# Kernel tuning notes

Measured on AMD Instinct MI355X. Metric: run time of the kernel, lower is better.

Reference implementation:

```python
import jax, jax.numpy as jnp
import numpy as np

B, H, W, C = 2, 48, 96, 128
N = H * W
NH, HD = 8, 32
WIN_R = 1
WLEN = 2 * WIN_R + 2
ATTN_NUM = WLEN * WLEN
FIELD_DIM = 2
D_SELF = C + FIELD_DIM + NH * 2   # 146
E_SELF = D_SELF + 1               # 147 (noc embed)
D_CROSS = C + FIELD_DIM           # 130
ATTN_DIM = NH * HD                # 256
HID = C * 2                       # ConvGLU hidden
SCALE = HD ** -0.5


def init_coords():
    gx, gy = jnp.meshgrid(jnp.arange(W, dtype=jnp.float32), jnp.arange(H, dtype=jnp.float32))
    return jnp.stack([gx, gy], axis=-1)[None]  # [1,H,W,2] (x,y)


def layer_norm(x, g, b, eps=1e-5):
    mu = x.mean(-1, keepdims=True)
    var = ((x - mu) ** 2).mean(-1, keepdims=True)
    return (x - mu) * jax.lax.rsqrt(var + eps) * g + b


def swap_halves(t):
    a, b = jnp.split(t, 2, axis=0)
    return jnp.concatenate([b, a], axis=0)


def bilinear_sample(img, coords):
    # img [B,H,W,C]; coords [B,H,W,2] absolute (x,y)
    x = jnp.clip(coords[..., 0], 0.0, W - 1.0)
    y = jnp.clip(coords[..., 1], 0.0, H - 1.0)
    x0 = jnp.clip(jnp.floor(x), 0, W - 2).astype(jnp.int32); x1 = x0 + 1
    y0 = jnp.clip(jnp.floor(y), 0, H - 2).astype(jnp.int32); y1 = y0 + 1
    wx = (x - x0)[..., None]; wy = (y - y0)[..., None]
    bi = jnp.arange(img.shape[0])[:, None, None]
    v00 = img[bi, y0, x0]; v01 = img[bi, y0, x1]
    v10 = img[bi, y1, x0]; v11 = img[bi, y1, x1]
    return (1 - wy) * ((1 - wx) * v00 + wx * v01) + wy * ((1 - wx) * v10 + wx * v11)


def consistency_mask(field, A=2.0):
    offset = field + init_coords()
    f_t2r = bilinear_sample(swap_halves(field), offset)
    diff = jnp.abs(field + f_t2r).sum(-1, keepdims=True)
    return (diff < A).astype(field.dtype)  # [B,H,W,1]


def match_attention_core(q, k, v, max_offset):
    # q,k,v: [B,N,NH,HD]; max_offset: [B,N,NH,2] absolute (x,y)
    r = WIN_R
    ox = jnp.clip(max_offset[..., 0], float(r), W - 1 - r - 0.001)
    oy = jnp.clip(max_offset[..., 1], float(r), H - 1 - r - 0.001)
    mxf = jnp.floor(ox); myf = jnp.floor(oy)
    fx = (ox - mxf).transpose(0, 2, 1)[..., None, None]  # [B,NH,N,1,1]
    fy = (oy - myf).transpose(0, 2, 1)[..., None, None]
    mx = mxf.astype(jnp.int32).transpose(0, 2, 1)  # [B,NH,N]
    my = myf.astype(jnp.int32).transpose(0, 2, 1)
    qh = q.transpose(0, 2, 1, 3); kh = k.transpose(0, 2, 1, 3); vh = v.transpose(0, 2, 1, 3)
    dxs = jnp.arange(WLEN) - r                    # window: floor-r .. floor+r+1
    gx = mx[..., None] + dxs                      # [B,NH,N,WLEN]
    gy = my[..., None] + dxs
    idx = (gy[..., :, None] * W + gx[..., None, :]).reshape(B, NH, N, ATTN_NUM)
    bi = jnp.arange(B)[:, None, None, None]
    hi = jnp.arange(NH)[None, :, None, None]
    kg = kh[bi, hi, idx]                          # [B,NH,N,ATTN_NUM,HD]
    s = jnp.einsum('bhnd,bhnad->bhna', qh, kg) * SCALE
    S = s.reshape(B, NH, N, WLEN, WLEN)           # [..., y, x]
    w00 = (1 - fy) * (1 - fx); w01 = (1 - fy) * fx; w10 = fy * (1 - fx); w11 = fy * fx
    # continuous (2r+1)^2 window scores by bilinear interp of integer-grid scores
    s_cont = (w00 * S[..., :-1, :-1] + w01 * S[..., :-1, 1:]
              + w10 * S[..., 1:, :-1] + w11 * S[..., 1:, 1:])
    p = jax.nn.softmax(s_cont.reshape(B, NH, N, -1), axis=-1).reshape(s_cont.shape)
    # scatter continuous probs back to the (2r+2)^2 integer grid with bilinear weights
    Ag = jnp.zeros((B, NH, N, WLEN, WLEN), p.dtype)
    Ag = Ag.at[..., :-1, :-1].add(w00 * p)
    Ag = Ag.at[..., :-1, 1:].add(w01 * p)
    Ag = Ag.at[..., 1:, :-1].add(w10 * p)
    Ag = Ag.at[..., 1:, 1:].add(w11 * p)
    Af = Ag.reshape(B, NH, N, ATTN_NUM)
    vg = vh[bi, hi, idx]                          # [B,NH,N,ATTN_NUM,HD]
    out = jnp.einsum('bhna,bhnad->bhnd', Af, vg)
    return out.transpose(0, 2, 1, 3).reshape(B, N, ATTN_DIM), Af.transpose(0, 2, 1, 3)


def reference(x, self_rpos, field, field_scale, n0_g, n0_b, n1_g, n1_b, n2_g, n2_b,
              sq_w, sk_w, sv_w, sp_w, cq_w, ck_w, cv_w, cg_w, cp_w,
              fc1_w, fc1_b, dw_w, dw_b, fc2_w, fc2_b):
    noc = consistency_mask(jax.lax.stop_gradient(field))
    xc = jnp.concatenate([x, field * field_scale, self_rpos], axis=-1)  # [B,H,W,D_SELF]
    coords0 = jnp.tile(init_coords(), (1, 1, 1, NH))  # [1,H,W,2*NH]
    self_off = (self_rpos + coords0).reshape(B, N, NH, 2)
    # --- self MatchAttention (noc_embed) ---
    h0 = layer_norm(xc, n0_g, n0_b).reshape(B, N, D_SELF)
    xe = jnp.concatenate([h0, noc.reshape(B, N, 1)], axis=-1)
    q = (xe @ sq_w).reshape(B, N, NH, HD)
    k = (xe @ sk_w).reshape(B, N, NH, HD)
    v = (xe @ sv_w).reshape(B, N, NH, HD)
    o, _ = match_attention_core(q, k, v, self_off)
    xc = xc + (o @ sp_w).reshape(B, H, W, D_SELF)
    self_rpos_out = xc[..., -NH * 2:]
    xc = xc[..., :D_CROSS]
    xc = xc.at[..., -1].set(0.0)  # stereo: zero y-flow
    field1 = xc[..., -FIELD_DIM:] / field_scale
    off = (jnp.tile(field1, (1, 1, 1, NH)) + coords0).reshape(B, N, NH, 2)
    # --- cross MatchAttention ---
    h1 = layer_norm(xc, n1_g, n1_b).reshape(B, N, D_CROSS)
    ref = h1
    tgt = swap_halves(h1)
    g = jax.nn.silu(ref @ cg_w)
    q = (ref @ cq_w).reshape(B, N, NH, HD)
    k = (tgt @ ck_w).reshape(B, N, NH, HD)
    v = (tgt @ cv_w).reshape(B, N, NH, HD)
    o, attn = match_attention_core(q, k, v, off)
    o = jnp.concatenate([g * o, attn.reshape(B, N, NH * ATTN_NUM)], axis=-1)
    xc = xc + (o @ cp_w).reshape(B, H, W, D_CROSS)
    xc = xc.at[..., -1].set(0.0)
    field2 = xc[..., -FIELD_DIM:] / field_scale
    xo = xc[..., :C]
    # --- ConvGLU MLP ---
    h2 = layer_norm(xo, n2_g, n2_b)
    u = h2 @ fc1_w + fc1_b
    a, gv = jnp.split(u, 2, axis=-1)
    a = jax.lax.conv_general_dilated(a, dw_w, (1, 1), 'SAME',
                                     dimension_numbers=('NHWC', 'HWIO', 'NHWC'),
                                     feature_group_count=HID) + dw_b
    a = jax.nn.gelu(a, approximate=False) * gv
    xo = xo + (a @ fc2_w + fc2_b)
    return xo, self_rpos_out, field2


def setup_inputs() -> dict:
    key = jax.random.key(0)
    ks = jax.random.split(key, 16)
    def rn(i, shape, s=1.0):
        return jax.random.normal(ks[i], shape, dtype=jnp.float32) * s
    return {
        'x': rn(0, (B, H, W, C)),
        'self_rpos': rn(1, (B, H, W, NH * 2)),
        'field': rn(2, (B, H, W, FIELD_DIM)),
        'field_scale': 0.1 * jnp.ones((1, 1, 1, 2), jnp.float32),
        'n0_g': jnp.ones((D_SELF,), jnp.float32), 'n0_b': jnp.zeros((D_SELF,), jnp.float32),
        'n1_g': jnp.ones((D_CROSS,), jnp.float32), 'n1_b': jnp.zeros((D_CROSS,), jnp.float32),
        'n2_g': jnp.ones((C,), jnp.float32), 'n2_b': jnp.zeros((C,), jnp.float32),
        'sq_w': rn(3, (E_SELF, ATTN_DIM), 0.02), 'sk_w': rn(4, (E_SELF, ATTN_DIM), 0.02),
        'sv_w': rn(5, (E_SELF, ATTN_DIM), 0.02), 'sp_w': rn(6, (ATTN_DIM, D_SELF), 0.02),
        'cq_w': rn(7, (D_CROSS, ATTN_DIM), 0.02), 'ck_w': rn(8, (D_CROSS, ATTN_DIM), 0.02),
        'cv_w': rn(9, (D_CROSS, ATTN_DIM), 0.02), 'cg_w': rn(10, (D_CROSS, ATTN_DIM), 0.02),
        'cp_w': rn(11, (ATTN_DIM + NH * ATTN_NUM, D_CROSS), 0.02),
        'fc1_w': rn(12, (C, 2 * HID), 0.02), 'fc1_b': jnp.zeros((2 * HID,), jnp.float32),
        'dw_w': rn(13, (3, 3, 1, HID), 0.1), 'dw_b': jnp.zeros((HID,), jnp.float32),
        'fc2_w': rn(14, (HID, C), 0.02), 'fc2_b': jnp.zeros((C,), jnp.float32),
    }
```

## Files before the change

### kernel.cpp

```cpp
#include <hip/hip_runtime.h>
#include <math.h>

namespace {
constexpr int Bn = 2, Hh = 48, Ww = 96, Cch = 128;
constexpr int Nn = Hh * Ww;
constexpr int NHh = 8;
constexpr int DSELF = 146, ESELF = 147, DCROSS = 130;
constexpr int Mrows = Bn * Nn;
constexpr float SCALEf = 0.17677669529663687f;
}

typedef float f32x4 __attribute__((ext_vector_type(4)));
typedef short s16x8 __attribute__((ext_vector_type(8)));

__device__ __forceinline__ unsigned short f2b(float f) {
  unsigned int u = __float_as_uint(f);
  u = u + 0x7fffu + ((u >> 16) & 1u);
  return (unsigned short)(u >> 16);
}
__device__ __forceinline__ float b2f(unsigned short u) {
  return __uint_as_float((unsigned int)u << 16);
}

__device__ __forceinline__ f32x4 mfma_bf16(s16x8 a, s16x8 b, f32x4 c) {
  f32x4 d;
  asm volatile("v_mfma_f32_16x16x32_bf16 %0, %1, %2, %3"
               : "=&v"(d) : "v"(a), "v"(b), "v"(c));
  return d;
}

__device__ __forceinline__ float wave_bcast_sum(float v) {
#pragma unroll
  for (int off = 32; off > 0; off >>= 1) v += __shfl_down(v, off);
  return __shfl(v, 0);
}

struct WDesc { const float* src; int K, N, Kp, dstOff, blkOff; };
struct WPack { WDesc d[11]; };

__global__ __launch_bounds__(256) void convert_w_kernel(WPack p, unsigned short* dst) {
  int bi = blockIdx.x;
  int mi = 0;
#pragma unroll
  for (int i = 1; i < 11; i++) if (bi >= p.d[i].blkOff) mi = i;
  WDesc w = p.d[mi];
  int e = (bi - w.blkOff) * 2048 + threadIdx.x * 8;
  int total = w.N * w.Kp;
  if (e >= total) return;
  int n = e / w.Kp, k0 = e - n * w.Kp;
  s16x8 pack;
#pragma unroll
  for (int j = 0; j < 8; j++) {
    int kk = k0 + j;
    float vv = (kk < w.K) ? w.src[(size_t)kk * w.N + n] : 0.f;
    pack[j] = (short)f2b(vv);
  }
  *reinterpret_cast<s16x8*>(dst + w.dstOff + e) = pack;
}

__global__ __launch_bounds__(256) void mfma_gemm_kernel(
    const unsigned short* __restrict__ A, int Kp,
    const unsigned short* __restrict__ Wt, int N,
    const float* __restrict__ bias, const float* __restrict__ resid,
    void* __restrict__ out, int swapA, int act, int out_bf16) {
  __shared__ unsigned short As[64 * 40];
  __shared__ unsigned short Bs[64 * 40];
  int tid = threadIdx.x;
  int m0 = blockIdx.y * 64, n0 = blockIdx.x * 64;
  int lane = tid & 63, wv = tid >> 6;
  int wr = wv >> 1, wc = wv & 1;
  int lr = lane & 15, lk = (lane >> 4) * 8;
  int sr = tid >> 2, sk8 = (tid & 3) * 8;
  int am = m0 + sr;
  if (swapA) am = (am < Mrows / 2) ? am + Mrows / 2 : am - Mrows / 2;
  const unsigned short* aptr = A + (size_t)am * Kp + sk8;
  int bn = n0 + sr;
  const unsigned short* bptr = (bn < N) ? Wt + (size_t)bn * Kp + sk8 : nullptr;
  f32x4 acc00 = {}, acc01 = {}, acc10 = {}, acc11 = {};
  for (int k0 = 0; k0 < Kp; k0 += 32) {
    s16x8 av = *reinterpret_cast<const s16x8*>(aptr + k0);
    s16x8 bv = {};
    if (bptr) bv = *reinterpret_cast<const s16x8*>(bptr + k0);
    *reinterpret_cast<s16x8*>(&As[sr * 40 + sk8]) = av;
    *reinterpret_cast<s16x8*>(&Bs[sr * 40 + sk8]) = bv;
    __syncthreads();
    s16x8 a0 = *reinterpret_cast<const s16x8*>(&As[(wr * 32 + lr) * 40 + lk]);
    s16x8 a1 = *reinterpret_cast<const s16x8*>(&As[(wr * 32 + 16 + lr) * 40 + lk]);
    s16x8 b0 = *reinterpret_cast<const s16x8*>(&Bs[(wc * 32 + lr) * 40 + lk]);
    s16x8 b1 = *reinterpret_cast<const s16x8*>(&Bs[(wc * 32 + 16 + lr) * 40 + lk]);
    acc00 = mfma_bf16(a0, b0, acc00);
    acc01 = mfma_bf16(a0, b1, acc01);
    acc10 = mfma_bf16(a1, b0, acc10);
    acc11 = mfma_bf16(a1, b1, acc11);
    __syncthreads();
  }
  int rowBase = m0 + wr * 32 + (lane >> 4) * 4;
  f32x4 accs[2][2] = {{acc00, acc01}, {acc10, acc11}};
#pragma unroll
  for (int fc = 0; fc < 2; fc++) {
    int col = n0 + wc * 32 + fc * 16 + lr;
    if (col >= N) continue;
    float bval = bias ? bias[col] : 0.f;
    bool dosilu = (act == 1) || (act == 2 && col >= 256);
#pragma unroll
    for (int fr = 0; fr < 2; fr++) {
#pragma unroll
      for (int r = 0; r < 4; r++) {
        int row = rowBase + fr * 16 + r;
        float vv = accs[fr][fc][r] + bval;
        if (resid) vv += resid[(size_t)row * N + col];
        if (dosilu) vv = vv / (1.f + expf(-vv));
        if (out_bf16)
          ((unsigned short*)out)[(size_t)row * N + col] = f2b(vv);
        else
          ((float*)out)[(size_t)row * N + col] = vv;
      }
    }
  }
}

__global__ __launch_bounds__(256) void prep_kernel(
    const float* __restrict__ x, const float* __restrict__ rpos,
    const float* __restrict__ field, const float* __restrict__ fs,
    const float* __restrict__ n0g, const float* __restrict__ n0b,
    float* __restrict__ xc, unsigned short* __restrict__ xe_b) {
  int wv = threadIdx.x >> 6, lane = threadIdx.x & 63;
  int pix = blockIdx.x * 4 + wv;
  int b = pix / Nn, n = pix - b * Nn;
  int py = n / Ww, px = n - py * Ww;
  const float* xrow = x + (size_t)pix * Cch;
  const float* rrow = rpos + (size_t)pix * 16;
  float f0 = field[(size_t)pix * 2 + 0], f1 = field[(size_t)pix * 2 + 1];
  float fsx = fs[0], fsy = fs[1];
  float vals[3];
#pragma unroll
  for (int i = 0; i < 3; i++) {
    int c = lane + i * 64;
    float v = 0.f;
    if (c < Cch) v = xrow[c];
    else if (c == 128) v = f0 * fsx;
    else if (c == 129) v = f1 * fsy;
    else if (c < DSELF) v = rrow[c - 130];
    vals[i] = v;
  }
  float* xcrow = xc + (size_t)pix * DSELF;
#pragma unroll
  for (int i = 0; i < 3; i++) {
    int c = lane + i * 64;
    if (c < DSELF) xcrow[c] = vals[i];
  }
  float s = 0.f;
#pragma unroll
  for (int i = 0; i < 3; i++) { int c = lane + i * 64; if (c < DSELF) s += vals[i]; }
  float mu = wave_bcast_sum(s) * (1.f / DSELF);
  float s2 = 0.f;
#pragma unroll
  for (int i = 0; i < 3; i++) {
    int c = lane + i * 64;
    if (c < DSELF) { float d = vals[i] - mu; s2 += d * d; }
  }
  float var = wave_bcast_sum(s2) * (1.f / DSELF);
  float rs = rsqrtf(var + 1e-5f);
  float noc = 0.f;
  if (lane == 0) {
    float ox = fminf(fmaxf(f0 + (float)px, 0.f), (float)(Ww - 1));
    float oy = fminf(fmaxf(f1 + (float)py, 0.f), (float)(Hh - 1));
    float x0f = fminf(fmaxf(floorf(ox), 0.f), (float)(Ww - 2));
    float y0f = fminf(fmaxf(floorf(oy), 0.f), (float)(Hh - 2));
    int x0 = (int)x0f, y0 = (int)y0f;
    float wx = ox - x0f, wy = oy - y0f;
    const float* fo = field + (size_t)(1 - b) * Nn * 2;
    const float* p00 = fo + ((size_t)y0 * Ww + x0) * 2;
    const float* p10 = fo + ((size_t)(y0 + 1) * Ww + x0) * 2;
    float v0 = (1.f - wy) * ((1.f - wx) * p00[0] + wx * p00[2]) +
               wy * ((1.f - wx) * p10[0] + wx * p10[2]);
    float v1 = (1.f - wy) * ((1.f - wx) * p00[1] + wx * p00[3]) +
               wy * ((1.f - wx) * p10[1] + wx * p10[3]);
    float diff = fabsf(f0 + v0) + fabsf(f1 + v1);
    noc = (diff < 2.f) ? 1.f : 0.f;
  }
  noc = __shfl(noc, 0);
  unsigned short* xerow = xe_b + (size_t)pix * 160;
#pragma unroll
  for (int i = 0; i < 3; i++) {
    int c = lane + i * 64;
    if (c < 160) {
      float v;
      if (c < DSELF) v = (vals[i] - mu) * rs * n0g[c] + n0b[c];
      else if (c == 146) v = noc;
      else v = 0.f;
      xerow[c] = f2b(v);
    }
  }
}

__global__ __launch_bounds__(256) void attn_wave_kernel(
    const float* __restrict__ qbuf, int qstride, int gOff,
    const float* __restrict__ kvbuf, int kvstride, int koff, int voff,
    const float* __restrict__ rpos, const float* __restrict__ xc2,
    const float* __restrict__ fs, unsigned short* __restrict__ o, int o_stride,
    int mode) {
  int wv = threadIdx.x >> 6, lane = threadIdx.x & 63;
  int pix = blockIdx.x * 4 + wv;
  int b = pix / Nn, n = pix - b * Nn;
  int py = n / Ww, px = n - py * Ww;
  int h = lane >> 3, c = lane & 7;
  size_t row = (size_t)pix;
  float ox, oy;
  if (mode == 0) {
    ox = rpos[row * 16 + 2 * h] + (float)px;
    oy = rpos[row * 16 + 2 * h + 1] + (float)py;
  } else {
    ox = xc2[row * DCROSS + 128] / fs[0] + (float)px;
    oy = (float)py;
  }
  ox = fminf(fmaxf(ox, 1.0f), 93.999f);
  oy = fminf(fmaxf(oy, 1.0f), 45.999f);
  float mxf = floorf(ox), myf = floorf(oy);
  float fx = ox - mxf, fy = oy - myf;
  int mx = (int)mxf, my = (int)myf;
  int base = b * Nn;

  float4 qv = *reinterpret_cast<const float4*>(qbuf + row * qstride + lane * 4);
  float s[16];
#pragma unroll
  for (int j = 0; j < 4; j++) {
    int gy = my - 1 + j;
#pragma unroll
    for (int i = 0; i < 4; i++) {
      int gx = mx - 1 + i;
      int idx = gy * Ww + gx;
      float4 kv = *reinterpret_cast<const float4*>(
          kvbuf + (size_t)(base + idx) * kvstride + koff + lane * 4);
      float d = qv.x * kv.x + qv.y * kv.y + qv.z * kv.z + qv.w * kv.w;
      d += __shfl_xor(d, 1);
      d += __shfl_xor(d, 2);
      d += __shfl_xor(d, 4);
      s[j * 4 + i] = d * SCALEf;
    }
  }
  float w00 = (1.f - fy) * (1.f - fx), w01 = (1.f - fy) * fx;
  float w10 = fy * (1.f - fx), w11 = fy * fx;
  float sc[9];
#pragma unroll
  for (int j = 0; j < 3; j++)
#pragma unroll
    for (int i = 0; i < 3; i++)
      sc[j * 3 + i] = w00 * s[j * 4 + i] + w01 * s[j * 4 + i + 1] +
                      w10 * s[(j + 1) * 4 + i] + w11 * s[(j + 1) * 4 + i + 1];
  float mval = sc[0];
#pragma unroll
  for (int i = 1; i < 9; i++) mval = fmaxf(mval, sc[i]);
  float p[9], psum = 0.f;
#pragma unroll
  for (int i = 0; i < 9; i++) { p[i] = expf(sc[i] - mval); psum += p[i]; }
  float inv = 1.f / psum;
#pragma unroll
  for (int i = 0; i < 9; i++) p[i] *= inv;
  float Ag[16] = {};
#pragma unroll
  for (int j = 0; j < 3; j++)
#pragma unroll
    for (int i = 0; i < 3; i++) {
      float pv = p[j * 3 + i];
      Ag[j * 4 + i] += w00 * pv;
      Ag[j * 4 + i + 1] += w01 * pv;
      Ag[(j + 1) * 4 + i] += w10 * pv;
      Ag[(j + 1) * 4 + i + 1] += w11 * pv;
    }
  float4 acc = make_float4(0.f, 0.f, 0.f, 0.f);
#pragma unroll
  for (int j = 0; j < 4; j++) {
    int gy = my - 1 + j;
#pragma unroll
    for (int i = 0; i < 4; i++) {
      int gx = mx - 1 + i;
      int idx = gy * Ww + gx;
      float4 vv = *reinterpret_cast<const float4*>(
          kvbuf + (size_t)(base + idx) * kvstride + voff + lane * 4);
      float w = Ag[j * 4 + i];
      acc.x += w * vv.x; acc.y += w * vv.y; acc.z += w * vv.z; acc.w += w * vv.w;
    }
  }
  if (gOff >= 0) {
    float4 gg = *reinterpret_cast<const float4*>(qbuf + row * qstride + gOff + lane * 4);
    acc.x *= gg.x; acc.y *= gg.y; acc.z *= gg.z; acc.w *= gg.w;
  }
  unsigned int p0 = (unsigned int)f2b(acc.x) | ((unsigned int)f2b(acc.y) << 16);
  unsigned int p1 = (unsigned int)f2b(acc.z) | ((unsigned int)f2b(acc.w) << 16);
  *reinterpret_cast<uint2*>(o + row * o_stride + lane * 4) = make_uint2(p0, p1);
  if (mode == 1) {
    float a0 = 0.f, a1 = 0.f;
#pragma unroll
    for (int a = 0; a < 8; a++) {
      if (c == a) { a0 = Ag[2 * a]; a1 = Ag[2 * a + 1]; }
    }
    unsigned int pa = (unsigned int)f2b(a0) | ((unsigned int)f2b(a1) << 16);
    *reinterpret_cast<unsigned int*>(o + row * o_stride + 256 + h * 16 + 2 * c) = pa;
  }
}

__global__ __launch_bounds__(256) void post_self_kernel(
    const float* __restrict__ xcn, const float* __restrict__ n1g,
    const float* __restrict__ n1b, float* __restrict__ out_rpos,
    float* __restrict__ xc2, unsigned short* __restrict__ h1_b) {
  int wv = threadIdx.x >> 6, lane = threadIdx.x & 63;
  int pix = blockIdx.x * 4 + wv;
  const float* row = xcn + (size_t)pix * DSELF;
  float vals[3];
#pragma unroll
  for (int i = 0; i < 3; i++) {
    int c = lane + i * 64;
    vals[i] = (c < DSELF) ? row[c] : 0.f;
  }
#pragma unroll
  for (int i = 0; i < 3; i++) {
    int c = lane + i * 64;
    if (c >= 130 && c < 146) out_rpos[(size_t)pix * 16 + (c - 130)] = vals[i];
  }
#pragma unroll
  for (int i = 0; i < 3; i++) {
    int c = lane + i * 64;
    if (c == 129) vals[i] = 0.f;
  }
  float* x2row = xc2 + (size_t)pix * DCROSS;
#pragma unroll
  for (int i = 0; i < 3; i++) {
    int c = lane + i * 64;
    if (c < DCROSS) x2row[c] = vals[i];
  }
  float s = 0.f;
#pragma unroll
  for (int i = 0; i < 3; i++) { int c = lane + i * 64; if (c < DCROSS) s += vals[i]; }
  float mu = wave_bcast_sum(s) * (1.f / DCROSS);
  float s2 = 0.f;
#pragma unroll
  for (int i = 0; i < 3; i++) {
    int c = lane + i * 64;
    if (c < DCROSS) { float d = vals[i] - mu; s2 += d * d; }
  }
  float var = wave_bcast_sum(s2) * (1.f / DCROSS);
  float rs = rsqrtf(var + 1e-5f);
  unsigned short* h1row = h1_b + (size_t)pix * 160;
#pragma unroll
  for (int i = 0; i < 3; i++) {
    int c = lane + i * 64;
    if (c < 160) {
      float v = (c < DCROSS) ? (vals[i] - mu) * rs * n1g[c] + n1b[c] : 0.f;
      h1row[c] = f2b(v);
    }
  }
}

__global__ __launch_bounds__(256) void post_cross_kernel(
    const float* __restrict__ xc2n, const float* __restrict__ fs,
    const float* __restrict__ n2g, const float* __restrict__ n2b,
    float* __restrict__ out_f2, float* __restrict__ xob,
    unsigned short* __restrict__ h2_b) {
  int wv = threadIdx.x >> 6, lane = threadIdx.x & 63;
  int pix = blockIdx.x * 4 + wv;
  const float* row = xc2n + (size_t)pix * DCROSS;
  float vals[3];
#pragma unroll
  for (int i = 0; i < 3; i++) {
    int c = lane + i * 64;
    vals[i] = (c < DCROSS) ? row[c] : 0.f;
  }
  if (lane == 0) out_f2[(size_t)pix * 2 + 0] = vals[2] / fs[0];
  if (lane == 1) out_f2[(size_t)pix * 2 + 1] = 0.f;
  float* xrow = xob + (size_t)pix * Cch;
#pragma unroll
  for (int i = 0; i < 2; i++) {
    int c = lane + i * 64;
    xrow[c] = vals[i];
  }
  float s = vals[0] + vals[1];
  float mu = wave_bcast_sum(s) * (1.f / Cch);
  float d0 = vals[0] - mu, d1 = vals[1] - mu;
  float var = wave_bcast_sum(d0 * d0 + d1 * d1) * (1.f / Cch);
  float rs = rsqrtf(var + 1e-5f);
  unsigned short* h2row = h2_b + (size_t)pix * Cch;
#pragma unroll
  for (int i = 0; i < 2; i++) {
    int c = lane + i * 64;
    h2row[c] = f2b((vals[i] - mu) * rs * n2g[c] + n2b[c]);
  }
}

__global__ __launch_bounds__(256) void dwconv_kernel(
    const unsigned short* __restrict__ ub, const float* __restrict__ dww,
    const float* __restrict__ dwb, unsigned short* __restrict__ aout) {
  int t = blockIdx.x * 256 + threadIdx.x;
  int c8 = (t & 31) * 8;
  int pix = t >> 5;
  int b = pix / Nn, n = pix - b * Nn;
  int py = n / Ww, px = n - py * Ww;
  float acc[8];
#pragma unroll
  for (int j = 0; j < 8; j++) acc[j] = dwb[c8 + j];
#pragma unroll
  for (int ky = 0; ky < 3; ky++) {
    int yy = py + ky - 1;
    if (yy < 0 || yy >= Hh) continue;
#pragma unroll
    for (int kx = 0; kx < 3; kx++) {
      int xx = px + kx - 1;
      if (xx < 0 || xx >= Ww) continue;
      s16x8 uv = *reinterpret_cast<const s16x8*>(
          ub + ((size_t)(b * Nn + yy * Ww + xx)) * 512 + c8);
      const float* wrow = dww + (ky * 3 + kx) * 256 + c8;
#pragma unroll
      for (int j = 0; j < 8; j++)
        acc[j] += b2f((unsigned short)uv[j]) * wrow[j];
    }
  }
  s16x8 gate = *reinterpret_cast<const s16x8*>(ub + (size_t)pix * 512 + 256 + c8);
  s16x8 outp;
#pragma unroll
  for (int j = 0; j < 8; j++) {
    float a = acc[j];
    float ge = 0.5f * a * (1.f + erff(a * 0.70710678118654752f));
    outp[j] = (short)f2b(ge * b2f((unsigned short)gate[j]));
  }
  *reinterpret_cast<s16x8*>(aout + (size_t)pix * 256 + c8) = outp;
}

extern "C" void kernel_launch(void* const* d_in, const int* in_sizes, int n_in,
                              void* d_out, int out_size, void* d_ws, size_t ws_size,
                              hipStream_t stream) {
  (void)in_sizes; (void)n_in; (void)out_size; (void)ws_size;
  const float* x    = (const float*)d_in[0];
  const float* rpos = (const float*)d_in[1];
  const float* field= (const float*)d_in[2];
  const float* fs   = (const float*)d_in[3];
  const float* n0g  = (const float*)d_in[4];
  const float* n0b  = (const float*)d_in[5];
  const float* n1g  = (const float*)d_in[6];
  const float* n1b  = (const float*)d_in[7];
  const float* n2g  = (const float*)d_in[8];
  const float* n2b  = (const float*)d_in[9];
  const float* sq_w = (const float*)d_in[10];
  const float* sk_w = (const float*)d_in[11];
  const float* sv_w = (const float*)d_in[12];
  const float* sp_w = (const float*)d_in[13];
  const float* cq_w = (const float*)d_in[14];
  const float* ck_w = (const float*)d_in[15];
  const float* cv_w = (const float*)d_in[16];
  const float* cg_w = (const float*)d_in[17];
  const float* cp_w = (const float*)d_in[18];
  const float* fc1w = (const float*)d_in[19];
  const float* fc1b = (const float*)d_in[20];
  const float* dww  = (const float*)d_in[21];
  const float* dwb  = (const float*)d_in[22];
  const float* fc2w = (const float*)d_in[23];
  const float* fc2b = (const float*)d_in[24];

  float* ws = (float*)d_ws;
  float* xc    = ws + 0;
  float* xcn   = ws + 1345536;
  float* xc2   = ws + 2691072;
  float* xc2n  = ws + 3889152;
  float* xob   = ws + 5087232;
  unsigned short* xe_b   = (unsigned short*)(ws + 6266880);
  unsigned short* h1_b   = (unsigned short*)(ws + 7004160);
  unsigned short* h2_b   = (unsigned short*)(ws + 7741440);
  float* qkv   = ws + 8331264;
  float* qg    = ws + 15409152;
  float* kv    = ws + 20127744;
  unsigned short* o_b    = (unsigned short*)(ws + 24846336);
  unsigned short* ocat_b = (unsigned short*)(ws + 26025984);
  unsigned short* warena = (unsigned short*)(ws + 27795456);
  unsigned short* u_b    = (unsigned short*)qkv;
  unsigned short* aconv_b = o_b;

  float* out_xo   = (float*)d_out;
  float* out_rpos = out_xo + 1179648;
  float* out_f2   = out_xo + 1327104;

  const int oSQKV = 0;
  const int oSP   = 122880;
  const int oCQG  = 160256;
  const int oCKV  = 242176;
  const int oCP   = 324096;
  const int oF1   = 374016;
  const int oF2   = 439552;
  WPack wp;
  auto setw = [&](int i, const float* src, int K, int N, int Kp, int off) {
    wp.d[i].src = src; wp.d[i].K = K; wp.d[i].N = N; wp.d[i].Kp = Kp;
    wp.d[i].dstOff = off;
  };
  setw(0, sq_w, 147, 256, 160, oSQKV);
  setw(1, sk_w, 147, 256, 160, oSQKV + 40960);
  setw(2, sv_w, 147, 256, 160, oSQKV + 81920);
  setw(3, sp_w, 256, 146, 256, oSP);
  setw(4, cq_w, 130, 256, 160, oCQG);
  setw(5, cg_w, 130, 256, 160, oCQG + 40960);
  setw(6, ck_w, 130, 256, 160, oCKV);
  setw(7, cv_w, 130, 256, 160, oCKV + 40960);
  setw(8, cp_w, 384, 130, 384, oCP);
  setw(9, fc1w, 128, 512, 128, oF1);
  setw(10, fc2w, 256, 128, 256, oF2);
  int nblk = 0;
  for (int i = 0; i < 11; i++) {
    wp.d[i].blkOff = nblk;
    nblk += (wp.d[i].N * wp.d[i].Kp + 2047) / 2048;
  }

  dim3 blk(256);
  auto gemm = [&](const unsigned short* A, int Kp, int woff, int N,
                  const float* bias, const float* resid, void* out,
                  int swapA, int act, int obf) {
    dim3 grid((N + 63) / 64, Mrows / 64);
    mfma_gemm_kernel<<<grid, blk, 0, stream>>>(A, Kp, warena + woff, N, bias,
                                               resid, out, swapA, act, obf);
  };

  convert_w_kernel<<<nblk, blk, 0, stream>>>(wp, warena);
  prep_kernel<<<2304, blk, 0, stream>>>(x, rpos, field, fs, n0g, n0b, xc, xe_b);
  gemm(xe_b, 160, oSQKV, 768, nullptr, nullptr, qkv, 0, 0, 0);
  attn_wave_kernel<<<2304, blk, 0, stream>>>(qkv, 768, -1, qkv, 768, 256, 512,
                                             rpos, nullptr, fs, o_b, 256, 0);
  gemm(o_b, 256, oSP, 146, nullptr, xc, xcn, 0, 0, 0);
  post_self_kernel<<<2304, blk, 0, stream>>>(xcn, n1g, n1b, out_rpos, xc2, h1_b);
  gemm(h1_b, 160, oCQG, 512, nullptr, nullptr, qg, 0, 2, 0);
  gemm(h1_b, 160, oCKV, 512, nullptr, nullptr, kv, 1, 0, 0);
  attn_wave_kernel<<<2304, blk, 0, stream>>>(qg, 512, 256, kv, 512, 0, 256,
                                             nullptr, xc2, fs, ocat_b, 384, 1);
  gemm(ocat_b, 384, oCP, 130, nullptr, xc2, xc2n, 0, 0, 0);
  post_cross_kernel<<<2304, blk, 0, stream>>>(xc2n, fs, n2g, n2b, out_f2, xob, h2_b);
  gemm(h2_b, 128, oF1, 512, fc1b, nullptr, u_b, 0, 0, 1);
  dwconv_kernel<<<1152, blk, 0, stream>>>(u_b, dww, dwb, aconv_b);
  gemm(aconv_b, 256, oF2, 128, fc2b, xob, out_xo, 0, 0, 0);
}
```

Measured before the change: 161.9 us.

## Add 32-row GEMM tile for narrow outputs and fuse weight conversion into prep

```diff
diff --git a/kernel.cpp b/kernel.cpp
--- a/kernel.cpp
+++ b/kernel.cpp
@@ -38,8 +38,8 @@
 struct WDesc { const float* src; int K, N, Kp, dstOff, blkOff; };
 struct WPack { WDesc d[11]; };
 
-__global__ __launch_bounds__(256) void convert_w_kernel(WPack p, unsigned short* dst) {
-  int bi = blockIdx.x;
+__device__ __forceinline__ void convert_w_body(const WPack& p, unsigned short* dst,
+                                               int bi) {
   int mi = 0;
 #pragma unroll
   for (int i = 1; i < 11; i++) if (bi >= p.d[i].blkOff) mi = i;
@@ -119,13 +119,81 @@
   }
 }
 
+__global__ __launch_bounds__(128) void mfma_gemm32_kernel(
+    const unsigned short* __restrict__ A, int Kp,
+    const unsigned short* __restrict__ Wt, int N,
+    const float* __restrict__ bias, const float* __restrict__ resid,
+    void* __restrict__ out, int swapA, int act, int out_bf16) {
+  __shared__ unsigned short As[32 * 40];
+  __shared__ unsigned short Bs[64 * 40];
+  int tid = threadIdx.x;
+  int m0 = blockIdx.y * 32, n0 = blockIdx.x * 64;
+  int lane = tid & 63, wv = tid >> 6;
+  int lr = lane & 15, lk = (lane >> 4) * 8;
+  int sr = tid >> 2, sk8 = (tid & 3) * 8;
+  int am = m0 + sr;
+  if (swapA) am = (am < Mrows / 2) ? am + Mrows / 2 : am - Mrows / 2;
+  const unsigned short* aptr = A + (size_t)am * Kp + sk8;
+  int bn0 = n0 + sr, bn1 = n0 + sr + 32;
+  const unsigned short* bptr0 = (bn0 < N) ? Wt + (size_t)bn0 * Kp + sk8 : nullptr;
+  const unsigned short* bptr1 = (bn1 < N) ? Wt + (size_t)bn1 * Kp + sk8 : nullptr;
+  f32x4 acc00 = {}, acc01 = {}, acc10 = {}, acc11 = {};
+  for (int k0 = 0; k0 < Kp; k0 += 32) {
+    s16x8 av = *reinterpret_cast<const s16x8*>(aptr + k0);
+    s16x8 bv0 = {}, bv1 = {};
+    if (bptr0) bv0 = *reinterpret_cast<const s16x8*>(bptr0 + k0);
+    if (bptr1) bv1 = *reinterpret_cast<const s16x8*>(bptr1 + k0);
+    *reinterpret_cast<s16x8*>(&As[sr * 40 + sk8]) = av;
+    *reinterpret_cast<s16x8*>(&Bs[sr * 40 + sk8]) = bv0;
+    *reinterpret_cast<s16x8*>(&Bs[(sr + 32) * 40 + sk8]) = bv1;
+    __syncthreads();
+    s16x8 a0 = *reinterpret_cast<const s16x8*>(&As[lr * 40 + lk]);
+    s16x8 a1 = *reinterpret_cast<const s16x8*>(&As[(16 + lr) * 40 + lk]);
+    s16x8 b0 = *reinterpret_cast<const s16x8*>(&Bs[(wv * 32 + lr) * 40 + lk]);
+    s16x8 b1 = *reinterpret_cast<const s16x8*>(&Bs[(wv * 32 + 16 + lr) * 40 + lk]);
+    acc00 = mfma_bf16(a0, b0, acc00);
+    acc01 = mfma_bf16(a0, b1, acc01);
+    acc10 = mfma_bf16(a1, b0, acc10);
+    acc11 = mfma_bf16(a1, b1, acc11);
+    __syncthreads();
+  }
+  int rowBase = m0 + (lane >> 4) * 4;
+  f32x4 accs[2][2] = {{acc00, acc01}, {acc10, acc11}};
+#pragma unroll
+  for (int fc = 0; fc < 2; fc++) {
+    int col = n0 + wv * 32 + fc * 16 + lr;
+    if (col >= N) continue;
+    float bval = bias ? bias[col] : 0.f;
+    bool dosilu = (act == 1) || (act == 2 && col >= 256);
+#pragma unroll
+    for (int fr = 0; fr < 2; fr++) {
+#pragma unroll
+      for (int r = 0; r < 4; r++) {
+        int row = rowBase + fr * 16 + r;
+        float vv = accs[fr][fc][r] + bval;
+        if (resid) vv += resid[(size_t)row * N + col];
+        if (dosilu) vv = vv / (1.f + expf(-vv));
+        if (out_bf16)
+          ((unsigned short*)out)[(size_t)row * N + col] = f2b(vv);
+        else
+          ((float*)out)[(size_t)row * N + col] = vv;
+      }
+    }
+  }
+}
+
 __global__ __launch_bounds__(256) void prep_kernel(
+    WPack wp, unsigned short* __restrict__ warena, int nconv,
     const float* __restrict__ x, const float* __restrict__ rpos,
     const float* __restrict__ field, const float* __restrict__ fs,
     const float* __restrict__ n0g, const float* __restrict__ n0b,
     float* __restrict__ xc, unsigned short* __restrict__ xe_b) {
+  if (blockIdx.x < (unsigned)nconv) {
+    convert_w_body(wp, warena, blockIdx.x);
+    return;
+  }
   int wv = threadIdx.x >> 6, lane = threadIdx.x & 63;
-  int pix = blockIdx.x * 4 + wv;
+  int pix = (blockIdx.x - nconv) * 4 + wv;
   int b = pix / Nn, n = pix - b * Nn;
   int py = n / Ww, px = n - py * Ww;
   const float* xrow = x + (size_t)pix * Cch;
@@ -510,13 +578,19 @@
   auto gemm = [&](const unsigned short* A, int Kp, int woff, int N,
                   const float* bias, const float* resid, void* out,
                   int swapA, int act, int obf) {
-    dim3 grid((N + 63) / 64, Mrows / 64);
-    mfma_gemm_kernel<<<grid, blk, 0, stream>>>(A, Kp, warena + woff, N, bias,
-                                               resid, out, swapA, act, obf);
+    if (N <= 384) {
+      dim3 grid((N + 63) / 64, Mrows / 32);
+      mfma_gemm32_kernel<<<grid, dim3(128), 0, stream>>>(
+          A, Kp, warena + woff, N, bias, resid, out, swapA, act, obf);
+    } else {
+      dim3 grid((N + 63) / 64, Mrows / 64);
+      mfma_gemm_kernel<<<grid, blk, 0, stream>>>(
+          A, Kp, warena + woff, N, bias, resid, out, swapA, act, obf);
+    }
   };
 
-  convert_w_kernel<<<nblk, blk, 0, stream>>>(wp, warena);
-  prep_kernel<<<2304, blk, 0, stream>>>(x, rpos, field, fs, n0g, n0b, xc, xe_b);
+  prep_kernel<<<nblk + 2304, blk, 0, stream>>>(wp, warena, nblk, x, rpos, field,
+                                               fs, n0g, n0b, xc, xe_b);
   gemm(xe_b, 160, oSQKV, 768, nullptr, nullptr, qkv, 0, 0, 0);
   attn_wave_kernel<<<2304, blk, 0, stream>>>(qkv, 768, -1, qkv, 768, 256, 512,
                                              rpos, nullptr, fs, o_b, 256, 0);
```

Result: no change. 160.9 us (-0.6%).
